# Kernel tuning notes

Hardware: AMD Instinct MI355X
Metric: run time of the kernel (lower is better)

The kernel has to match this reference:

```python
import jax, jax.numpy as jnp
import numpy as np

B, S, HID = 1, 2048, 7168
QLORA = 1536
NH = 32          # index_n_heads
HD = 128         # index_head_dim
ROPE = 64        # qk_rope_head_dim
TOPK = 512       # index_topk
EPS = 1e-6
NEG = -1e9       # finite mask value -> deterministic top-k (no -inf ties)


def _rope(x, cos, sin):
    # non-interleaved rotary: x [b,s,h,d]; cos/sin [s, d//2]
    half = x.shape[-1] // 2
    x1, x2 = x[..., :half], x[..., half:]
    c = cos[None, :, None, :]
    s = sin[None, :, None, :]
    return jnp.concatenate([x1 * c - x2 * s, x1 * s + x2 * c], axis=-1)


def setup_inputs() -> dict:
    key = jax.random.key(0)
    ks = jax.random.split(key, 8)
    x = jax.random.normal(ks[0], (B, S, HID), jnp.float32)
    qr = jax.random.normal(ks[1], (B, S, QLORA), jnp.float32)
    # rotary tables, theta=10000
    inv = 1.0 / (10000.0 ** (np.arange(0, ROPE, 2, dtype=np.float32) / ROPE))
    ang = np.arange(S, dtype=np.float32)[:, None] * inv[None, :]   # [S, ROPE//2]
    freqs_cos = jnp.asarray(np.cos(ang))
    freqs_sin = jnp.asarray(np.sin(ang))
    # causal additive mask [S, S], broadcasts over batch on [b,t,s]
    tri = jnp.tril(jnp.ones((S, S), jnp.bool_))
    mask = jnp.where(tri, 0.0, NEG).astype(jnp.float32)
    wq_b = jax.random.normal(ks[2], (QLORA, NH * HD), jnp.float32) / np.sqrt(QLORA)
    wk = jax.random.normal(ks[3], (HID, HD), jnp.float32) / np.sqrt(HID)
    k_norm_w = jnp.ones((HD,), jnp.float32)
    w_weights = jax.random.normal(ks[4], (HID, NH), jnp.float32) / np.sqrt(HID)
    return {"x": x, "qr": qr, "freqs_cos": freqs_cos, "freqs_sin": freqs_sin,
            "mask": mask, "wq_b": wq_b, "wk": wk, "k_norm_w": k_norm_w,
            "w_weights": w_weights}


def reference(x, qr, freqs_cos, freqs_sin, mask, wq_b, wk, k_norm_w, w_weights):
    b, s, _ = x.shape
    # queries
    q = (qr @ wq_b).reshape(b, s, NH, HD)
    q_pe, q_nope = q[..., :ROPE], q[..., ROPE:]
    q_pe = _rope(q_pe, freqs_cos, freqs_sin)
    q = jnp.concatenate([q_pe, q_nope], axis=-1)            # [b,s,NH,HD]
    # keys: project + RMSNorm + rope on first ROPE dims
    k = x @ wk                                              # [b,s,HD]
    var = jnp.mean(k * k, axis=-1, keepdims=True)
    k = k_norm_w * (k * jax.lax.rsqrt(var + EPS))
    k_pe, k_nope = k[..., :ROPE], k[..., ROPE:]
    k_pe = _rope(k_pe[:, :, None, :], freqs_cos, freqs_sin)[:, :, 0, :]
    k = jnp.concatenate([k_pe, k_nope], axis=-1)            # [b,s,HD]
    # per-head query weights
    weights = (x @ w_weights) * (NH ** -0.5) * (HD ** -0.5)  # [b,s,NH]
    # relu scores and per-head weighted reduction
    logits = jax.nn.relu(jnp.einsum('bthd,bsd->btsh', q, k))  # [b,t,s,NH]
    score = jnp.einsum('btsh,bth->bts', logits, weights) + mask
    # top-k token selection -> additive index mask
    topk_idx = jax.lax.top_k(score, min(TOPK, s))[1]          # [b,t,k]
    bi = jnp.arange(b)[:, None, None]
    ti = jnp.arange(s)[None, :, None]
    out = jnp.full((b, s, s), -jnp.inf, dtype=x.dtype)
    out = out.at[bi, ti, topk_idx].set(0.0)
    return out
```

## Files before the change

kernel.cpp:

```cpp
#include <hip/hip_runtime.h>
#include <hip/hip_bf16.h>
#include <math.h>

#define S_LEN 2048
#define HID   7168
#define QLORA 1536
#define NH    32
#define HD    128
#define T0    512
#define MROWS 1536
#define NEGV  -1000000000.0f
#define EPSV  1e-6f
#define NEG_FILL -3.0e38f
#define KSPLIT 16
#define KCHUNK 448

typedef __attribute__((ext_vector_type(8))) short bf16x8;
typedef __attribute__((ext_vector_type(4))) float f32x4;

__device__ __forceinline__ unsigned short f2bf(float x) {
    __hip_bfloat16 h = __float2bfloat16(x);
    union { __hip_bfloat16 h; unsigned short u; } cv; cv.h = h; return cv.u;
}
__device__ __forceinline__ float bf2f(short u) {
    return __uint_as_float(((unsigned)(unsigned short)u) << 16);
}
__device__ __forceinline__ void gload_lds16(const void* gsrc, void* ldst) {
    __builtin_amdgcn_global_load_lds(
        (const __attribute__((address_space(1))) void*)gsrc,
        (__attribute__((address_space(3))) void*)ldst,
        16, 0, 0);
}

__global__ __launch_bounds__(256) void prep(
    const float* __restrict__ wk, const float* __restrict__ ww,
    const float* __restrict__ wq_b,
    unsigned short* __restrict__ wbT, unsigned short* __restrict__ wqbT)
{
    __shared__ float tbuf[64][65];
    const int tid = threadIdx.x;
    const int b = blockIdx.x;
    if (b < 560) {
        const int k0 = (b % 112) * 64;
        const int nt = b / 112;
        const float* src; int ld, nc0;
        if (nt < 4) { src = wk; ld = HD; nc0 = nt * 32; }
        else        { src = ww; ld = NH; nc0 = 0; }
        {
            int r = tid >> 2, c0 = (tid & 3) * 8;
            const float* sp = &src[(size_t)(k0 + r) * ld + nc0 + c0];
            #pragma unroll
            for (int i = 0; i < 2; ++i) {
                float4 v = *(const float4*)(sp + 4 * i);
                tbuf[r][c0 + 4 * i]     = v.x;
                tbuf[r][c0 + 4 * i + 1] = v.y;
                tbuf[r][c0 + 4 * i + 2] = v.z;
                tbuf[r][c0 + 4 * i + 3] = v.w;
            }
        }
        __syncthreads();
        {
            int nn = tid >> 3, ks = (tid & 7) * 8;
            bf16x8 p;
            #pragma unroll
            for (int j = 0; j < 8; ++j) p[j] = (short)f2bf(tbuf[ks + j][nn]);
            *(bf16x8*)&wbT[(size_t)(nt * 32 + nn) * HID + k0 + ks] = p;
        }
    } else {
        const int b2 = b - 560;
        const int n0 = (b2 & 63) * 64;
        const int k0 = (b2 >> 6) * 64;
        {
            int r = tid >> 2, c0 = (tid & 3) * 16;
            const float* src = &wq_b[(size_t)(k0 + r) * 4096 + n0 + c0];
            #pragma unroll
            for (int i = 0; i < 4; ++i) {
                float4 v = *(const float4*)(src + 4 * i);
                tbuf[r][c0 + 4 * i]     = v.x;
                tbuf[r][c0 + 4 * i + 1] = v.y;
                tbuf[r][c0 + 4 * i + 2] = v.z;
                tbuf[r][c0 + 4 * i + 3] = v.w;
            }
        }
        __syncthreads();
        {
            int nn = tid >> 2, ks = (tid & 3) * 16;
            bf16x8 p0, p1;
            #pragma unroll
            for (int j = 0; j < 8; ++j) {
                p0[j] = (short)f2bf(tbuf[ks + j][nn]);
                p1[j] = (short)f2bf(tbuf[ks + 8 + j][nn]);
            }
            unsigned short* dst = &wqbT[(size_t)(n0 + nn) * QLORA + k0 + ks];
            *(bf16x8*)dst       = p0;
            *(bf16x8*)(dst + 8) = p1;
        }
    }
}

__global__ __launch_bounds__(256) void cast_qr(
    const float* __restrict__ qr, unsigned short* __restrict__ qrb)
{
    int idx = blockIdx.x * 256 + threadIdx.x;
    const float* src = qr + (size_t)T0 * QLORA + (size_t)idx * 8;
    float4 f0 = *(const float4*)src;
    float4 f1 = *(const float4*)(src + 4);
    bf16x8 p;
    p[0]=(short)f2bf(f0.x); p[1]=(short)f2bf(f0.y); p[2]=(short)f2bf(f0.z); p[3]=(short)f2bf(f0.w);
    p[4]=(short)f2bf(f1.x); p[5]=(short)f2bf(f1.y); p[6]=(short)f2bf(f1.z); p[7]=(short)f2bf(f1.w);
    *(bf16x8*)(qrb + (size_t)idx * 8) = p;
}

__global__ __launch_bounds__(256) void kw_gemm2(
    const float* __restrict__ x, const unsigned short* __restrict__ wbT,
    unsigned short* __restrict__ P)
{
    __shared__ char As[2][4096];
    __shared__ char Bs[2][10240];
    const int tid = threadIdx.x;
    const int bid = blockIdx.x;
    const int wg = (bid & 7) * 64 + (bid >> 3);
    const int kc = wg >> 5;
    const int m0 = (wg & 31) * 64;
    const int kbase = kc * KCHUNK;
    const int wv = tid >> 6, l = tid & 63, g = l >> 4, r15 = l & 15;
    const int ar = tid >> 2, asub = tid & 3;
    f32x4 acc[10] = {};
    float4 fa, fb;

#define LOAD_A(kt) do {                                                          \
        const float* ap = &x[(size_t)(m0 + ar) * HID + kbase + (kt) * 32 + asub * 8]; \
        fa = *(const float4*)ap;  fb = *(const float4*)(ap + 4);                 \
    } while (0)
#define WRITE_A(buf) do {                                                        \
        bf16x8 pk;                                                               \
        pk[0]=(short)f2bf(fa.x); pk[1]=(short)f2bf(fa.y);                        \
        pk[2]=(short)f2bf(fa.z); pk[3]=(short)f2bf(fa.w);                        \
        pk[4]=(short)f2bf(fb.x); pk[5]=(short)f2bf(fb.y);                        \
        pk[6]=(short)f2bf(fb.z); pk[7]=(short)f2bf(fb.w);                        \
        *(bf16x8*)(As[buf] + (ar << 6) + ((asub ^ ((ar >> 1) & 3)) << 4)) = pk;  \
    } while (0)
#define STAGE_B(buf, kt) do {                                                    \
        int k0_ = kbase + (kt) * 32;                                             \
        { int slot = (wv << 6) + l;                                              \
          int n_ = slot >> 2, sub_ = (slot & 3) ^ ((n_ >> 1) & 3);               \
          gload_lds16(wbT + (size_t)n_ * HID + k0_ + sub_ * 8,                   \
                      Bs[buf] + (wv << 10)); }                                   \
        { int slot = 256 + (wv << 6) + l;                                        \
          int n_ = slot >> 2, sub_ = (slot & 3) ^ ((n_ >> 1) & 3);               \
          gload_lds16(wbT + (size_t)n_ * HID + k0_ + sub_ * 8,                   \
                      Bs[buf] + 4096 + (wv << 10)); }                            \
        if (wv < 2) {                                                            \
          int slot = 512 + (wv << 6) + l;                                        \
          int n_ = slot >> 2, sub_ = (slot & 3) ^ ((n_ >> 1) & 3);               \
          gload_lds16(wbT + (size_t)n_ * HID + k0_ + sub_ * 8,                   \
                      Bs[buf] + 8192 + (wv << 10)); }                            \
    } while (0)

    LOAD_A(0);
    STAGE_B(0, 0);
    WRITE_A(0);
    __syncthreads();
    int cur = 0;
    for (int t = 0; t < 14; ++t) {
        if (t < 13) { LOAD_A(t + 1); STAGE_B(cur ^ 1, t + 1); }
        {
            char* Ab = As[cur];
            char* Bb = Bs[cur];
            int ra = (wv << 4) + r15;
            bf16x8 a = *(const bf16x8*)(Ab + (ra << 6) + ((g ^ ((ra >> 1) & 3)) << 4));
            #pragma unroll
            for (int fn = 0; fn < 10; ++fn) {
                int nb = (fn << 4) + r15;
                bf16x8 b = *(const bf16x8*)(Bb + (nb << 6) + ((g ^ ((nb >> 1) & 3)) << 4));
                acc[fn] = __builtin_amdgcn_mfma_f32_16x16x32_bf16(a, b, acc[fn], 0, 0, 0);
            }
        }
        if (t < 13) WRITE_A(cur ^ 1);
        __syncthreads();
        cur ^= 1;
    }
#undef LOAD_A
#undef WRITE_A
#undef STAGE_B
    #pragma unroll
    for (int fn = 0; fn < 10; ++fn)
        #pragma unroll
        for (int rr = 0; rr < 4; ++rr) {
            int row = m0 + (wv << 4) + (g << 2) + rr;
            P[((size_t)kc * S_LEN + row) * 160 + (fn << 4) + r15] = f2bf(acc[fn][rr]);
        }
}

__global__ __launch_bounds__(512) void kw_finish16(
    const unsigned short* __restrict__ P, const float* __restrict__ knw,
    const float* __restrict__ fcos, const float* __restrict__ fsin,
    unsigned short* __restrict__ Kf, float* __restrict__ W)
{
    __shared__ float res[16][160];
    __shared__ float rsq[16];
    const int tid = threadIdx.x;
    const int stile = blockIdx.x;
    const int row0 = stile * 16;
    const int r = tid >> 5, j = tid & 31;

    #pragma unroll
    for (int jj = 0; jj < 5; ++jj) {
        int c = j + 32 * jj;
        float s = 0.f;
        #pragma unroll
        for (int kc = 0; kc < KSPLIT; ++kc)
            s += bf2f((short)P[(size_t)(kc * S_LEN + row0 + r) * 160 + c]);
        res[r][c] = s;
    }
    __syncthreads();
    {
        float s2 = 0.f;
        #pragma unroll
        for (int cg = 0; cg < 4; ++cg) { float v = res[r][cg * 32 + j]; s2 += v * v; }
        #pragma unroll
        for (int off = 16; off > 0; off >>= 1) s2 += __shfl_xor(s2, off, 32);
        if (j == 0) rsq[r] = rsqrtf(s2 * (1.0f / 128.0f) + EPSV);
    }
    __syncthreads();
    {
        int rr = tid >> 5, h = tid & 31;
        W[(size_t)(row0 + rr) * NH + h] = res[rr][128 + h] * 0.015625f;
    }
    if (tid < 256) {
        int ks = tid >> 6, l = tid & 63;
        int row = l & 15, g = l >> 4;
        int t = row0 + row;
        float rs = rsq[row];
        bf16x8 pack;
        #pragma unroll
        for (int jj2 = 0; jj2 < 8; ++jj2) {
            int d = ks * 32 + 8 * g + jj2;
            float v;
            if (d < 32) {
                float a = res[row][d]      * rs * knw[d];
                float b = res[row][d + 32] * rs * knw[d + 32];
                v = a * fcos[(size_t)t * 32 + d] - b * fsin[(size_t)t * 32 + d];
            } else if (d < 64) {
                int jx = d - 32;
                float a = res[row][jx] * rs * knw[jx];
                float b = res[row][d]  * rs * knw[d];
                v = a * fsin[(size_t)t * 32 + jx] + b * fcos[(size_t)t * 32 + jx];
            } else {
                v = res[row][d] * rs * knw[d];
            }
            pack[jj2] = (short)f2bf(v);
        }
        *(bf16x8*)&Kf[(size_t)stile * 2048 + ks * 512 + l * 8] = pack;
    }
}

__global__ __launch_bounds__(256) void gemm_q2(
    const unsigned short* __restrict__ qrb, const unsigned short* __restrict__ wqbT,
    const float* __restrict__ fcos, const float* __restrict__ fsin,
    unsigned short* __restrict__ Qbu)
{
    __shared__ char lds[2][12288];
    const int tid = threadIdx.x;
    const int bid = blockIdx.x;
    const int wg = (bid & 7) * 96 + (bid >> 3);
    const int n0 = (wg / 24) * 128;
    const int m0 = (wg % 24) * 64;
    const int wv = tid >> 6, l = tid & 63, g = l >> 4, r15 = l & 15;
    const int lrow = l >> 2, lsub = l & 3;
    const int wm = wv >> 1, wn = wv & 1;
    f32x4 acc[2][4] = {};

#define STAGE_Q(buf, kt) do {                                                   \
        int k0_ = (kt) * 32;                                                    \
        { int row_ = wv * 16 + lrow; int gs_ = lsub ^ ((row_ >> 1) & 3);        \
          gload_lds16(qrb + (size_t)(m0 + row_) * QLORA + k0_ + gs_ * 8,        \
                      lds[buf] + (wv << 10)); }                                 \
        { int row_ = wv * 32 + lrow; int gs_ = lsub ^ ((row_ >> 1) & 3);        \
          gload_lds16(wqbT + (size_t)(n0 + row_) * QLORA + k0_ + gs_ * 8,       \
                      lds[buf] + 4096 + (wv << 11)); }                          \
        { int row_ = wv * 32 + 16 + lrow; int gs_ = lsub ^ ((row_ >> 1) & 3);   \
          gload_lds16(wqbT + (size_t)(n0 + row_) * QLORA + k0_ + gs_ * 8,       \
                      lds[buf] + 4096 + (wv << 11) + 1024); }                   \
    } while (0)

    STAGE_Q(0, 0);
    __syncthreads();
    int cur = 0;
    for (int t = 0; t < 48; ++t) {
        if (t + 1 < 48) STAGE_Q(cur ^ 1, t + 1);
        char* As = lds[cur];
        char* Bs = lds[cur] + 4096;
        bf16x8 a[2], b[4];
        #pragma unroll
        for (int fm = 0; fm < 2; ++fm) {
            int ra = wm * 32 + fm * 16 + r15;
            a[fm] = *(const bf16x8*)(As + (ra << 6) + ((g ^ ((ra >> 1) & 3)) << 4));
        }
        #pragma unroll
        for (int fn = 0; fn < 4; ++fn) {
            int nb = wn * 64 + fn * 16 + r15;
            b[fn] = *(const bf16x8*)(Bs + (nb << 6) + ((g ^ ((nb >> 1) & 3)) << 4));
        }
        #pragma unroll
        for (int fm = 0; fm < 2; ++fm)
            #pragma unroll
            for (int fn = 0; fn < 4; ++fn)
                acc[fm][fn] = __builtin_amdgcn_mfma_f32_16x16x32_bf16(a[fm], b[fn], acc[fm][fn], 0, 0, 0);
        __syncthreads();
        cur ^= 1;
    }
#undef STAGE_Q
    if (wn == 0) {
        #pragma unroll
        for (int fm = 0; fm < 2; ++fm)
            #pragma unroll
            for (int rr = 0; rr < 4; ++rr) {
                int t = T0 + m0 + wm * 32 + fm * 16 + 4 * g + rr;
                #pragma unroll
                for (int p = 0; p < 2; ++p) {
                    int jj = p * 16 + r15;
                    float c = fcos[(size_t)t * 32 + jj];
                    float s = fsin[(size_t)t * 32 + jj];
                    float a = acc[fm][p][rr], b = acc[fm][p + 2][rr];
                    acc[fm][p][rr]     = a * c - b * s;
                    acc[fm][p + 2][rr] = a * s + b * c;
                }
            }
    }
    #pragma unroll
    for (int fm = 0; fm < 2; ++fm)
        #pragma unroll
        for (int fn = 0; fn < 4; ++fn)
            #pragma unroll
            for (int rr = 0; rr < 4; ++rr) {
                int row = m0 + wm * 32 + fm * 16 + 4 * g + rr;
                int col = n0 + wn * 64 + fn * 16 + r15;
                Qbu[(size_t)row * 4096 + col] = f2bf(acc[fm][fn][rr]);
            }
}

__global__ __launch_bounds__(512, 2) void score_mfma3(
    const unsigned short* __restrict__ Qb, const unsigned short* __restrict__ Kf,
    const float* __restrict__ W, float* __restrict__ sc)
{
    __shared__ float ps[2][8][320];
    __shared__ float wl2[32][16];
    const int tid = threadIdx.x;
    const int tt  = 95 - blockIdx.x;
    const int sp  = blockIdx.y;
    const int t0  = T0 + 16 * tt;
    const int wv  = tid >> 6, l = tid & 63, g = l >> 4, r15 = l & 15;

    {
        int h = tid >> 4, gg = (tid >> 2) & 3, r = tid & 3;
        wl2[h][gg * 4 + r] = W[(size_t)(t0 + 4 * gg + r) * NH + h];
    }
    bf16x8 qf[4][4];
    {
        const unsigned short* qbase = Qb + (size_t)(16 * tt + r15) * 4096 + g * 8;
        #pragma unroll
        for (int hh = 0; hh < 4; ++hh)
            #pragma unroll
            for (int ks = 0; ks < 4; ++ks)
                qf[hh][ks] = *(const bf16x8*)(qbase + (4 * wv + hh) * 128 + ks * 32);
    }
    __syncthreads();

    const int nst = 33 + tt;
    bf16x8 kfc[4], kfn[4];
    if (sp < nst) {
        #pragma unroll
        for (int ks = 0; ks < 4; ++ks)
            kfc[ks] = *(const bf16x8*)&Kf[(size_t)sp * 2048 + ks * 512 + l * 8];
    }
    int pb = 0;
    for (int stile = sp; stile < nst; stile += 4) {
        if (stile + 4 < nst) {
            #pragma unroll
            for (int ks = 0; ks < 4; ++ks)
                kfn[ks] = *(const bf16x8*)&Kf[(size_t)(stile + 4) * 2048 + ks * 512 + l * 8];
        }
        f32x4 score = {0.f, 0.f, 0.f, 0.f};
        #pragma unroll
        for (int hh = 0; hh < 4; ++hh) {
            f32x4 acc = {0.f, 0.f, 0.f, 0.f};
            #pragma unroll
            for (int ks = 0; ks < 4; ++ks)
                acc = __builtin_amdgcn_mfma_f32_16x16x32_bf16(qf[hh][ks], kfc[ks], acc, 0, 0, 0);
            f32x4 w4 = *(const f32x4*)&wl2[4 * wv + hh][g * 4];
            #pragma unroll
            for (int r = 0; r < 4; ++r)
                score[r] += fmaxf(acc[r], 0.f) * w4[r];
        }
        #pragma unroll
        for (int r = 0; r < 4; ++r) ps[pb][wv][l * 5 + r] = score[r];
        __syncthreads();
        if (wv < 4) {
            float v = ps[pb][0][l * 5 + wv];
            #pragma unroll
            for (int w = 1; w < 8; ++w) v += ps[pb][w][l * 5 + wv];
            int t = t0 + 4 * g + wv;
            int s = stile * 16 + r15;
            sc[(size_t)(t - T0) * S_LEN + s] = (s <= t) ? v : NEGV;
        }
        #pragma unroll
        for (int ks = 0; ks < 4; ++ks) kfc[ks] = kfn[ks];
        pb ^= 1;
    }
}

__global__ __launch_bounds__(512) void topk_fill(
    const float* __restrict__ sc, float* __restrict__ out)
{
    __shared__ unsigned int hist[8][256];
    __shared__ unsigned int histT[256];
    __shared__ unsigned int wtot[8];
    __shared__ unsigned int sh_prefix;
    __shared__ int sh_krem;
    const int tid = threadIdx.x;
    if (blockIdx.x >= MROWS) {
        int idx = (blockIdx.x - MROWS) * 512 + tid;
        int col4 = idx & 511;
        float v = (col4 < 128) ? 0.0f : NEG_FILL;
        float4 o = {v, v, v, v};
        ((float4*)out)[idx] = o;
        return;
    }
    const int lane = tid & 63, wvi = tid >> 6;
    const int qrow = blockIdx.x;
    const int t = T0 + qrow;

    unsigned int uv[4];
    {
        float4 v = ((const float4*)(sc + (size_t)qrow * S_LEN))[tid];
        float vv[4] = {v.x, v.y, v.z, v.w};
        #pragma unroll
        for (int jj = 0; jj < 4; ++jj) {
            int i = tid * 4 + jj;
            float f = (i <= t) ? vv[jj] : NEGV;
            unsigned int b = __float_as_uint(f);
            uv[jj] = (b & 0x80000000u) ? ~b : (b | 0x80000000u);
        }
    }
    if (tid == 0) { sh_prefix = 0u; sh_krem = 512; }
    __syncthreads();

    #pragma unroll
    for (int pass = 0; pass < 4; ++pass) {
        const int shift = 24 - 8 * pass;
        ((unsigned int*)hist)[tid] = 0u;
        ((unsigned int*)hist)[tid + 512] = 0u;
        ((unsigned int*)hist)[tid + 1024] = 0u;
        ((unsigned int*)hist)[tid + 1536] = 0u;
        __syncthreads();
        unsigned int pfx = sh_prefix;
        #pragma unroll
        for (int jj = 0; jj < 4; ++jj) {
            bool ok = (pass == 0) || ((uv[jj] >> (shift + 8)) == (pfx >> (shift + 8)));
            if (ok) atomicAdd(&hist[wvi][(uv[jj] >> shift) & 255u], 1u);
        }
        __syncthreads();
        int krem = sh_krem;
        if (tid < 256) {
            unsigned int v = 0u;
            #pragma unroll
            for (int w = 0; w < 8; ++w) v += hist[w][tid];
            unsigned int s = v;
            #pragma unroll
            for (int off = 1; off < 64; off <<= 1) {
                unsigned int t2 = __shfl_down(s, off, 64);
                if (lane + off < 64) s += t2;
            }
            if (lane == 0) wtot[wvi] = s;
            histT[tid] = v;
        }
        __syncthreads();
        if (tid < 256) {
            unsigned int v = histT[tid];
            unsigned int s = v;
            #pragma unroll
            for (int off = 1; off < 64; off <<= 1) {
                unsigned int t2 = __shfl_down(s, off, 64);
                if (lane + off < 64) s += t2;
            }
            unsigned int S = s;
            #pragma unroll
            for (int w = 0; w < 4; ++w)
                if (w > wvi) S += wtot[w];
            if ((int)S >= krem && (int)(S - v) < krem) {
                sh_krem = krem - (int)(S - v);
                sh_prefix = pfx | ((unsigned int)tid << shift);
            }
        }
        __syncthreads();
    }

    const unsigned int uthr = sh_prefix;
    const int krem = sh_krem;
    int ec = 0;
    #pragma unroll
    for (int jj = 0; jj < 4; ++jj) ec += (uv[jj] == uthr) ? 1 : 0;
    unsigned int c = (unsigned int)ec;
    unsigned int p = c;
    #pragma unroll
    for (int off = 1; off < 64; off <<= 1) {
        unsigned int t2 = __shfl_up(p, off, 64);
        if (lane >= off) p += t2;
    }
    if (lane == 63) wtot[wvi] = p;
    __syncthreads();
    unsigned int add = 0;
    #pragma unroll
    for (int w = 0; w < 8; ++w)
        if (w < wvi) add += wtot[w];
    int base = (int)(p - c + add);

    float o[4];
    #pragma unroll
    for (int jj = 0; jj < 4; ++jj) {
        unsigned int u = uv[jj];
        bool sel;
        if (u > uthr) { sel = true; }
        else if (u == uthr) { sel = (base < krem); base++; }
        else { sel = false; }
        o[jj] = sel ? 0.0f : NEG_FILL;
    }
    float4 ov = {o[0], o[1], o[2], o[3]};
    ((float4*)(out + (size_t)t * S_LEN))[tid] = ov;
}

extern "C" void kernel_launch(void* const* d_in, const int* in_sizes, int n_in,
                              void* d_out, int out_size, void* d_ws, size_t ws_size,
                              hipStream_t stream)
{
    (void)in_sizes; (void)n_in; (void)out_size; (void)ws_size;
    const float* x    = (const float*)d_in[0];
    const float* qr   = (const float*)d_in[1];
    const float* fcos = (const float*)d_in[2];
    const float* fsin = (const float*)d_in[3];
    const float* wq_b = (const float*)d_in[5];
    const float* wk   = (const float*)d_in[6];
    const float* knw  = (const float*)d_in[7];
    const float* ww   = (const float*)d_in[8];
    float* out = (float*)d_out;
    char*  wsb = (char*)d_ws;

    unsigned short* Kf   = (unsigned short*)wsb;
    float*          W    = (float*)(wsb + 512 * 1024);
    unsigned short* wbT  = (unsigned short*)(wsb + 768 * 1024);
    unsigned short* wqbT = (unsigned short*)(wsb + 3080192);
    float*          sc   = (float*)(wsb + 3080192);
    unsigned short* qrb  = (unsigned short*)(wsb + 15663104);
    unsigned short* P    = (unsigned short*)(wsb + 15663104);
    unsigned short* Qbu  = (unsigned short*)d_out;

    prep        <<<2096, 256,        0, stream>>>(wk, ww, wq_b, wbT, wqbT);
    cast_qr     <<<1152, 256,        0, stream>>>(qr, qrb);
    gemm_q2     <<<768, 256,         0, stream>>>(qrb, wqbT, fcos, fsin, Qbu);
    kw_gemm2    <<<512, 256,         0, stream>>>(x, wbT, P);
    kw_finish16 <<<128, 512,         0, stream>>>(P, knw, fcos, fsin, Kf, W);
    score_mfma3 <<<dim3(96, 4), 512, 0, stream>>>(Qbu, Kf, W, sc);
    topk_fill   <<<2048, 512,        0, stream>>>(sc, out);
}
```

Measured before the change: 148.5 us.

## Triple-buffer Q-projection GEMM with manual vmcnt waits and single barrier

Converts the gemm_q2 main loop from double-buffered LDS staging with two syncthreads per step to a three-stage ring buffer. Each step uses explicit s_waitcnt vmcnt(3) plus one raw s_barrier, so two tiles of global-to-LDS loads stay in flight while the current one is computed. Global and LDS addresses are precomputed outside the loop and the loop is unrolled by three. This adds LDS (36KB per block) and may reduce occupancy, and it depends on precise vmcnt counting for correctness.

```diff
diff --git a/kernel.cpp b/kernel.cpp
--- a/kernel.cpp
+++ b/kernel.cpp
@@ -260,7 +260,7 @@
     const float* __restrict__ fcos, const float* __restrict__ fsin,
     unsigned short* __restrict__ Qbu)
 {
-    __shared__ char lds[2][12288];
+    __shared__ char lds[3][12288];
     const int tid = threadIdx.x;
     const int bid = blockIdx.x;
     const int wg = (bid & 7) * 96 + (bid >> 3);
@@ -271,46 +271,71 @@
     const int wm = wv >> 1, wn = wv & 1;
     f32x4 acc[2][4] = {};
 
-#define STAGE_Q(buf, kt) do {                                                   \
-        int k0_ = (kt) * 32;                                                    \
-        { int row_ = wv * 16 + lrow; int gs_ = lsub ^ ((row_ >> 1) & 3);        \
-          gload_lds16(qrb + (size_t)(m0 + row_) * QLORA + k0_ + gs_ * 8,        \
-                      lds[buf] + (wv << 10)); }                                 \
-        { int row_ = wv * 32 + lrow; int gs_ = lsub ^ ((row_ >> 1) & 3);        \
-          gload_lds16(wqbT + (size_t)(n0 + row_) * QLORA + k0_ + gs_ * 8,       \
-                      lds[buf] + 4096 + (wv << 11)); }                          \
-        { int row_ = wv * 32 + 16 + lrow; int gs_ = lsub ^ ((row_ >> 1) & 3);   \
-          gload_lds16(wqbT + (size_t)(n0 + row_) * QLORA + k0_ + gs_ * 8,       \
-                      lds[buf] + 4096 + (wv << 11) + 1024); }                   \
+    const int rowq = wv * 16 + lrow;
+    const char* gq  = (const char*)(qrb + (size_t)(m0 + rowq) * QLORA
+                                    + (lsub ^ ((rowq >> 1) & 3)) * 8);
+    const int  ldq  = wv << 10;
+    const int rowb1 = wv * 32 + lrow;
+    const char* gb1 = (const char*)(wqbT + (size_t)(n0 + rowb1) * QLORA
+                                    + (lsub ^ ((rowb1 >> 1) & 3)) * 8);
+    const int  ldb1 = 4096 + (wv << 11);
+    const int rowb2 = wv * 32 + 16 + lrow;
+    const char* gb2 = (const char*)(wqbT + (size_t)(n0 + rowb2) * QLORA
+                                    + (lsub ^ ((rowb2 >> 1) & 3)) * 8);
+    const int  ldb2 = 4096 + (wv << 11) + 1024;
+
+    const int ra0 = wm * 32 + r15,      ra1 = wm * 32 + 16 + r15;
+    const int offA0 = (ra0 << 6) + ((g ^ ((ra0 >> 1) & 3)) << 4);
+    const int offA1 = (ra1 << 6) + ((g ^ ((ra1 >> 1) & 3)) << 4);
+    const int nb0 = wn * 64 + r15,      nb1 = wn * 64 + 16 + r15;
+    const int nb2 = wn * 64 + 32 + r15, nb3 = wn * 64 + 48 + r15;
+    const int offB0 = 4096 + (nb0 << 6) + ((g ^ ((nb0 >> 1) & 3)) << 4);
+    const int offB1 = 4096 + (nb1 << 6) + ((g ^ ((nb1 >> 1) & 3)) << 4);
+    const int offB2 = 4096 + (nb2 << 6) + ((g ^ ((nb2 >> 1) & 3)) << 4);
+    const int offB3 = 4096 + (nb3 << 6) + ((g ^ ((nb3 >> 1) & 3)) << 4);
+
+#define STAGE3(bufi, kt) do {                                                   \
+        int kb = (kt) * 64;                                                     \
+        gload_lds16(gq  + kb, lds[bufi] + ldq);                                 \
+        gload_lds16(gb1 + kb, lds[bufi] + ldb1);                                \
+        gload_lds16(gb2 + kb, lds[bufi] + ldb2);                                \
     } while (0)
-
-    STAGE_Q(0, 0);
-    __syncthreads();
-    int cur = 0;
-    for (int t = 0; t < 48; ++t) {
-        if (t + 1 < 48) STAGE_Q(cur ^ 1, t + 1);
-        char* As = lds[cur];
-        char* Bs = lds[cur] + 4096;
-        bf16x8 a[2], b[4];
-        #pragma unroll
-        for (int fm = 0; fm < 2; ++fm) {
-            int ra = wm * 32 + fm * 16 + r15;
-            a[fm] = *(const bf16x8*)(As + (ra << 6) + ((g ^ ((ra >> 1) & 3)) << 4));
-        }
-        #pragma unroll
-        for (int fn = 0; fn < 4; ++fn) {
-            int nb = wn * 64 + fn * 16 + r15;
-            b[fn] = *(const bf16x8*)(Bs + (nb << 6) + ((g ^ ((nb >> 1) & 3)) << 4));
-        }
-        #pragma unroll
-        for (int fm = 0; fm < 2; ++fm)
-            #pragma unroll
-            for (int fn = 0; fn < 4; ++fn)
-                acc[fm][fn] = __builtin_amdgcn_mfma_f32_16x16x32_bf16(a[fm], b[fn], acc[fm][fn], 0, 0, 0);
-        __syncthreads();
-        cur ^= 1;
-    }
-#undef STAGE_Q
+#define COMPUTE(bufi) do {                                                      \
+        char* L_ = lds[bufi];                                                   \
+        bf16x8 a0 = *(const bf16x8*)(L_ + offA0);                               \
+        bf16x8 a1 = *(const bf16x8*)(L_ + offA1);                               \
+        bf16x8 b0_ = *(const bf16x8*)(L_ + offB0);                              \
+        bf16x8 b1_ = *(const bf16x8*)(L_ + offB1);                              \
+        bf16x8 b2_ = *(const bf16x8*)(L_ + offB2);                              \
+        bf16x8 b3_ = *(const bf16x8*)(L_ + offB3);                              \
+        acc[0][0] = __builtin_amdgcn_mfma_f32_16x16x32_bf16(a0, b0_, acc[0][0], 0, 0, 0); \
+        acc[0][1] = __builtin_amdgcn_mfma_f32_16x16x32_bf16(a0, b1_, acc[0][1], 0, 0, 0); \
+        acc[0][2] = __builtin_amdgcn_mfma_f32_16x16x32_bf16(a0, b2_, acc[0][2], 0, 0, 0); \
+        acc[0][3] = __builtin_amdgcn_mfma_f32_16x16x32_bf16(a0, b3_, acc[0][3], 0, 0, 0); \
+        acc[1][0] = __builtin_amdgcn_mfma_f32_16x16x32_bf16(a1, b0_, acc[1][0], 0, 0, 0); \
+        acc[1][1] = __builtin_amdgcn_mfma_f32_16x16x32_bf16(a1, b1_, acc[1][1], 0, 0, 0); \
+        acc[1][2] = __builtin_amdgcn_mfma_f32_16x16x32_bf16(a1, b2_, acc[1][2], 0, 0, 0); \
+        acc[1][3] = __builtin_amdgcn_mfma_f32_16x16x32_bf16(a1, b3_, acc[1][3], 0, 0, 0); \
+    } while (0)
+#define WAITV3 asm volatile("s_waitcnt vmcnt(3)" ::: "memory")
+#define WAITV0 asm volatile("s_waitcnt vmcnt(0)" ::: "memory")
+#define BAR    __builtin_amdgcn_s_barrier()
+
+    STAGE3(0, 0);
+    STAGE3(1, 1);
+    for (int t = 0; t < 45; t += 3) {
+        WAITV3; BAR; STAGE3(2, t + 2); COMPUTE(0);
+        WAITV3; BAR; STAGE3(0, t + 3); COMPUTE(1);
+        WAITV3; BAR; STAGE3(1, t + 4); COMPUTE(2);
+    }
+    WAITV3; BAR; STAGE3(2, 47); COMPUTE(0);
+    WAITV3; BAR; COMPUTE(1);
+    WAITV0; BAR; COMPUTE(2);
+#undef STAGE3
+#undef COMPUTE
+#undef WAITV3
+#undef WAITV0
+#undef BAR
     if (wn == 0) {
         #pragma unroll
         for (int fm = 0; fm < 2; ++fm)
```

New measurement: 147.2 us. Within noise of the previous version (-0.9%).

## Merge Q and K GEMMs into one launch, fuse qr cast, tweak score occupancy

Applied to the files above, without the earlier changes.

Combines the query GEMM and the key/weights GEMM into a single kernel whose blocks branch on block index, so both run concurrently in one launch. The separate qr fp32-to-bf16 cast kernel is removed; the query GEMM now loads fp32 qr and converts it in registers before writing to LDS, removing a kernel and a round trip through global memory. The score kernel switches to an explicit waves-per-EU attribute, loads the Q fragments with inline asm, and adds a sched_barrier. The shared LDS union sets occupancy for both halves, and the in-register conversion adds VALU work inside the Q GEMM loop.

```diff
diff --git a/kernel.cpp b/kernel.cpp
--- a/kernel.cpp
+++ b/kernel.cpp
@@ -98,98 +98,193 @@
     }
 }
 
-__global__ __launch_bounds__(256) void cast_qr(
-    const float* __restrict__ qr, unsigned short* __restrict__ qrb)
-{
-    int idx = blockIdx.x * 256 + threadIdx.x;
-    const float* src = qr + (size_t)T0 * QLORA + (size_t)idx * 8;
-    float4 f0 = *(const float4*)src;
-    float4 f1 = *(const float4*)(src + 4);
-    bf16x8 p;
-    p[0]=(short)f2bf(f0.x); p[1]=(short)f2bf(f0.y); p[2]=(short)f2bf(f0.z); p[3]=(short)f2bf(f0.w);
-    p[4]=(short)f2bf(f1.x); p[5]=(short)f2bf(f1.y); p[6]=(short)f2bf(f1.z); p[7]=(short)f2bf(f1.w);
-    *(bf16x8*)(qrb + (size_t)idx * 8) = p;
-}
-
-__global__ __launch_bounds__(256) void kw_gemm2(
+__global__ __launch_bounds__(256) void gemms(
+    const float* __restrict__ qr, const unsigned short* __restrict__ wqbT,
+    const float* __restrict__ fcos, const float* __restrict__ fsin,
+    unsigned short* __restrict__ Qbu,
     const float* __restrict__ x, const unsigned short* __restrict__ wbT,
     unsigned short* __restrict__ P)
 {
-    __shared__ char As[2][4096];
-    __shared__ char Bs[2][10240];
+    __shared__ char ldsu[28672];
     const int tid = threadIdx.x;
     const int bid = blockIdx.x;
-    const int wg = (bid & 7) * 64 + (bid >> 3);
-    const int kc = wg >> 5;
-    const int m0 = (wg & 31) * 64;
-    const int kbase = kc * KCHUNK;
     const int wv = tid >> 6, l = tid & 63, g = l >> 4, r15 = l & 15;
-    const int ar = tid >> 2, asub = tid & 3;
-    f32x4 acc[10] = {};
-    float4 fa, fb;
-
-#define LOAD_A(kt) do {                                                          \
-        const float* ap = &x[(size_t)(m0 + ar) * HID + kbase + (kt) * 32 + asub * 8]; \
+
+    if (bid < 768) {
+        const int wg = (bid & 7) * 96 + (bid >> 3);
+        const int n0 = (wg / 24) * 128;
+        const int m0 = (wg % 24) * 64;
+        const int wm = wv >> 1, wn = wv & 1;
+        const int ar = tid >> 2, asub = tid & 3;
+        f32x4 acc[2][4] = {};
+        float4 fa, fb;
+
+#define QA(buf)      (ldsu + (buf) * 4096)
+#define QB(buf)      (ldsu + 8192 + (buf) * 8192)
+#define LOAD_AQ(kt) do {                                                         \
+        const float* ap = &qr[(size_t)(T0 + m0 + ar) * QLORA + (kt) * 32 + asub * 8]; \
         fa = *(const float4*)ap;  fb = *(const float4*)(ap + 4);                 \
     } while (0)
-#define WRITE_A(buf) do {                                                        \
+#define WRITE_AQ(buf) do {                                                       \
         bf16x8 pk;                                                               \
         pk[0]=(short)f2bf(fa.x); pk[1]=(short)f2bf(fa.y);                        \
         pk[2]=(short)f2bf(fa.z); pk[3]=(short)f2bf(fa.w);                        \
         pk[4]=(short)f2bf(fb.x); pk[5]=(short)f2bf(fb.y);                        \
         pk[6]=(short)f2bf(fb.z); pk[7]=(short)f2bf(fb.w);                        \
-        *(bf16x8*)(As[buf] + (ar << 6) + ((asub ^ ((ar >> 1) & 3)) << 4)) = pk;  \
+        *(bf16x8*)(QA(buf) + (ar << 6) + ((asub ^ ((ar >> 1) & 3)) << 4)) = pk;  \
     } while (0)
-#define STAGE_B(buf, kt) do {                                                    \
+#define STAGE_BQ(buf, kt) do {                                                   \
+        int k0_ = (kt) * 32;                                                     \
+        { int slot = (wv << 6) + l;                                              \
+          int n_ = slot >> 2, sub_ = (slot & 3) ^ ((n_ >> 1) & 3);               \
+          gload_lds16(wqbT + (size_t)(n0 + n_) * QLORA + k0_ + sub_ * 8,         \
+                      QB(buf) + (wv << 10)); }                                   \
+        { int slot = 256 + (wv << 6) + l;                                        \
+          int n_ = slot >> 2, sub_ = (slot & 3) ^ ((n_ >> 1) & 3);               \
+          gload_lds16(wqbT + (size_t)(n0 + n_) * QLORA + k0_ + sub_ * 8,         \
+                      QB(buf) + 4096 + (wv << 10)); }                            \
+    } while (0)
+
+        LOAD_AQ(0);
+        STAGE_BQ(0, 0);
+        WRITE_AQ(0);
+        __syncthreads();
+        int cur = 0;
+        for (int t = 0; t < 48; ++t) {
+            if (t + 1 < 48) { LOAD_AQ(t + 1); STAGE_BQ(cur ^ 1, t + 1); }
+            {
+                char* Ab = QA(cur);
+                char* Bb = QB(cur);
+                bf16x8 a[2], b[4];
+                #pragma unroll
+                for (int fm = 0; fm < 2; ++fm) {
+                    int ra = wm * 32 + fm * 16 + r15;
+                    a[fm] = *(const bf16x8*)(Ab + (ra << 6) + ((g ^ ((ra >> 1) & 3)) << 4));
+                }
+                #pragma unroll
+                for (int fn = 0; fn < 4; ++fn) {
+                    int nb = wn * 64 + fn * 16 + r15;
+                    b[fn] = *(const bf16x8*)(Bb + (nb << 6) + ((g ^ ((nb >> 1) & 3)) << 4));
+                }
+                #pragma unroll
+                for (int fm = 0; fm < 2; ++fm)
+                    #pragma unroll
+                    for (int fn = 0; fn < 4; ++fn)
+                        acc[fm][fn] = __builtin_amdgcn_mfma_f32_16x16x32_bf16(a[fm], b[fn], acc[fm][fn], 0, 0, 0);
+            }
+            if (t + 1 < 48) WRITE_AQ(cur ^ 1);
+            __syncthreads();
+            cur ^= 1;
+        }
+#undef QA
+#undef QB
+#undef LOAD_AQ
+#undef WRITE_AQ
+#undef STAGE_BQ
+        if (wn == 0) {
+            #pragma unroll
+            for (int fm = 0; fm < 2; ++fm)
+                #pragma unroll
+                for (int rr = 0; rr < 4; ++rr) {
+                    int t = T0 + m0 + wm * 32 + fm * 16 + 4 * g + rr;
+                    #pragma unroll
+                    for (int p = 0; p < 2; ++p) {
+                        int jj = p * 16 + r15;
+                        float c = fcos[(size_t)t * 32 + jj];
+                        float s = fsin[(size_t)t * 32 + jj];
+                        float a = acc[fm][p][rr], b = acc[fm][p + 2][rr];
+                        acc[fm][p][rr]     = a * c - b * s;
+                        acc[fm][p + 2][rr] = a * s + b * c;
+                    }
+                }
+        }
+        #pragma unroll
+        for (int fm = 0; fm < 2; ++fm)
+            #pragma unroll
+            for (int fn = 0; fn < 4; ++fn)
+                #pragma unroll
+                for (int rr = 0; rr < 4; ++rr) {
+                    int row = m0 + wm * 32 + fm * 16 + 4 * g + rr;
+                    int col = n0 + wn * 64 + fn * 16 + r15;
+                    Qbu[(size_t)row * 4096 + col] = f2bf(acc[fm][fn][rr]);
+                }
+    } else {
+        const int bid2 = bid - 768;
+        const int wg = (bid2 & 7) * 64 + (bid2 >> 3);
+        const int kc = wg >> 5;
+        const int m0 = (wg & 31) * 64;
+        const int kbase = kc * KCHUNK;
+        const int ar = tid >> 2, asub = tid & 3;
+        f32x4 acc[10] = {};
+        float4 fa, fb;
+
+#define KA(buf)      (ldsu + (buf) * 4096)
+#define KB(buf)      (ldsu + 8192 + (buf) * 10240)
+#define LOAD_AK(kt) do {                                                         \
+        const float* ap = &x[(size_t)(m0 + ar) * HID + kbase + (kt) * 32 + asub * 8]; \
+        fa = *(const float4*)ap;  fb = *(const float4*)(ap + 4);                 \
+    } while (0)
+#define WRITE_AK(buf) do {                                                       \
+        bf16x8 pk;                                                               \
+        pk[0]=(short)f2bf(fa.x); pk[1]=(short)f2bf(fa.y);                        \
+        pk[2]=(short)f2bf(fa.z); pk[3]=(short)f2bf(fa.w);                        \
+        pk[4]=(short)f2bf(fb.x); pk[5]=(short)f2bf(fb.y);                        \
+        pk[6]=(short)f2bf(fb.z); pk[7]=(short)f2bf(fb.w);                        \
+        *(bf16x8*)(KA(buf) + (ar << 6) + ((asub ^ ((ar >> 1) & 3)) << 4)) = pk;  \
+    } while (0)
+#define STAGE_BK(buf, kt) do {                                                   \
         int k0_ = kbase + (kt) * 32;                                             \
         { int slot = (wv << 6) + l;                                              \
           int n_ = slot >> 2, sub_ = (slot & 3) ^ ((n_ >> 1) & 3);               \
           gload_lds16(wbT + (size_t)n_ * HID + k0_ + sub_ * 8,                   \
-                      Bs[buf] + (wv << 10)); }                                   \
+                      KB(buf) + (wv << 10)); }                                   \
         { int slot = 256 + (wv << 6) + l;                                        \
           int n_ = slot >> 2, sub_ = (slot & 3) ^ ((n_ >> 1) & 3);               \
           gload_lds16(wbT + (size_t)n_ * HID + k0_ + sub_ * 8,                   \
-                      Bs[buf] + 4096 + (wv << 10)); }                            \
+                      KB(buf) + 4096 + (wv << 10)); }                            \
         if (wv < 2) {                                                            \
           int slot = 512 + (wv << 6) + l;                                        \
           int n_ = slot >> 2, sub_ = (slot & 3) ^ ((n_ >> 1) & 3);               \
           gload_lds16(wbT + (size_t)n_ * HID + k0_ + sub_ * 8,                   \
-                      Bs[buf] + 8192 + (wv << 10)); }                            \
+                      KB(buf) + 8192 + (wv << 10)); }                            \
     } while (0)
 
-    LOAD_A(0);
-    STAGE_B(0, 0);
-    WRITE_A(0);
-    __syncthreads();
-    int cur = 0;
-    for (int t = 0; t < 14; ++t) {
-        if (t < 13) { LOAD_A(t + 1); STAGE_B(cur ^ 1, t + 1); }
-        {
-            char* Ab = As[cur];
-            char* Bb = Bs[cur];
-            int ra = (wv << 4) + r15;
-            bf16x8 a = *(const bf16x8*)(Ab + (ra << 6) + ((g ^ ((ra >> 1) & 3)) << 4));
-            #pragma unroll
-            for (int fn = 0; fn < 10; ++fn) {
-                int nb = (fn << 4) + r15;
-                bf16x8 b = *(const bf16x8*)(Bb + (nb << 6) + ((g ^ ((nb >> 1) & 3)) << 4));
-                acc[fn] = __builtin_amdgcn_mfma_f32_16x16x32_bf16(a, b, acc[fn], 0, 0, 0);
-            }
-        }
-        if (t < 13) WRITE_A(cur ^ 1);
-        __syncthreads();
-        cur ^= 1;
-    }
-#undef LOAD_A
-#undef WRITE_A
-#undef STAGE_B
-    #pragma unroll
-    for (int fn = 0; fn < 10; ++fn)
-        #pragma unroll
-        for (int rr = 0; rr < 4; ++rr) {
-            int row = m0 + (wv << 4) + (g << 2) + rr;
-            P[((size_t)kc * S_LEN + row) * 160 + (fn << 4) + r15] = f2bf(acc[fn][rr]);
-        }
+        LOAD_AK(0);
+        STAGE_BK(0, 0);
+        WRITE_AK(0);
+        __syncthreads();
+        int cur = 0;
+        for (int t = 0; t < 14; ++t) {
+            if (t < 13) { LOAD_AK(t + 1); STAGE_BK(cur ^ 1, t + 1); }
+            {
+                char* Ab = KA(cur);
+                char* Bb = KB(cur);
+                int ra = (wv << 4) + r15;
+                bf16x8 a = *(const bf16x8*)(Ab + (ra << 6) + ((g ^ ((ra >> 1) & 3)) << 4));
+                #pragma unroll
+                for (int fn = 0; fn < 10; ++fn) {
+                    int nb = (fn << 4) + r15;
+                    bf16x8 b = *(const bf16x8*)(Bb + (nb << 6) + ((g ^ ((nb >> 1) & 3)) << 4));
+                    acc[fn] = __builtin_amdgcn_mfma_f32_16x16x32_bf16(a, b, acc[fn], 0, 0, 0);
+                }
+            }
+            if (t < 13) WRITE_AK(cur ^ 1);
+            __syncthreads();
+            cur ^= 1;
+        }
+#undef KA
+#undef KB
+#undef LOAD_AK
+#undef WRITE_AK
+#undef STAGE_BK
+        #pragma unroll
+        for (int fn = 0; fn < 10; ++fn)
+            #pragma unroll
+            for (int rr = 0; rr < 4; ++rr) {
+                int row = m0 + (wv << 4) + (g << 2) + rr;
+                P[((size_t)kc * S_LEN + row) * 160 + (fn << 4) + r15] = f2bf(acc[fn][rr]);
+            }
+    }
 }
 
 __global__ __launch_bounds__(512) void kw_finish16(
@@ -255,92 +350,9 @@
     }
 }
 
-__global__ __launch_bounds__(256) void gemm_q2(
-    const unsigned short* __restrict__ qrb, const unsigned short* __restrict__ wqbT,
-    const float* __restrict__ fcos, const float* __restrict__ fsin,
-    unsigned short* __restrict__ Qbu)
-{
-    __shared__ char lds[2][12288];
-    const int tid = threadIdx.x;
-    const int bid = blockIdx.x;
-    const int wg = (bid & 7) * 96 + (bid >> 3);
-    const int n0 = (wg / 24) * 128;
-    const int m0 = (wg % 24) * 64;
-    const int wv = tid >> 6, l = tid & 63, g = l >> 4, r15 = l & 15;
-    const int lrow = l >> 2, lsub = l & 3;
-    const int wm = wv >> 1, wn = wv & 1;
-    f32x4 acc[2][4] = {};
-
-#define STAGE_Q(buf, kt) do {                                                   \
-        int k0_ = (kt) * 32;                                                    \
-        { int row_ = wv * 16 + lrow; int gs_ = lsub ^ ((row_ >> 1) & 3);        \
-          gload_lds16(qrb + (size_t)(m0 + row_) * QLORA + k0_ + gs_ * 8,        \
-                      lds[buf] + (wv << 10)); }                                 \
-        { int row_ = wv * 32 + lrow; int gs_ = lsub ^ ((row_ >> 1) & 3);        \
-          gload_lds16(wqbT + (size_t)(n0 + row_) * QLORA + k0_ + gs_ * 8,       \
-                      lds[buf] + 4096 + (wv << 11)); }                          \
-        { int row_ = wv * 32 + 16 + lrow; int gs_ = lsub ^ ((row_ >> 1) & 3);   \
-          gload_lds16(wqbT + (size_t)(n0 + row_) * QLORA + k0_ + gs_ * 8,       \
-                      lds[buf] + 4096 + (wv << 11) + 1024); }                   \
-    } while (0)
-
-    STAGE_Q(0, 0);
-    __syncthreads();
-    int cur = 0;
-    for (int t = 0; t < 48; ++t) {
-        if (t + 1 < 48) STAGE_Q(cur ^ 1, t + 1);
-        char* As = lds[cur];
-        char* Bs = lds[cur] + 4096;
-        bf16x8 a[2], b[4];
-        #pragma unroll
-        for (int fm = 0; fm < 2; ++fm) {
-            int ra = wm * 32 + fm * 16 + r15;
-            a[fm] = *(const bf16x8*)(As + (ra << 6) + ((g ^ ((ra >> 1) & 3)) << 4));
-        }
-        #pragma unroll
-        for (int fn = 0; fn < 4; ++fn) {
-            int nb = wn * 64 + fn * 16 + r15;
-            b[fn] = *(const bf16x8*)(Bs + (nb << 6) + ((g ^ ((nb >> 1) & 3)) << 4));
-        }
-        #pragma unroll
-        for (int fm = 0; fm < 2; ++fm)
-            #pragma unroll
-            for (int fn = 0; fn < 4; ++fn)
-                acc[fm][fn] = __builtin_amdgcn_mfma_f32_16x16x32_bf16(a[fm], b[fn], acc[fm][fn], 0, 0, 0);
-        __syncthreads();
-        cur ^= 1;
-    }
-#undef STAGE_Q
-    if (wn == 0) {
-        #pragma unroll
-        for (int fm = 0; fm < 2; ++fm)
-            #pragma unroll
-            for (int rr = 0; rr < 4; ++rr) {
-                int t = T0 + m0 + wm * 32 + fm * 16 + 4 * g + rr;
-                #pragma unroll
-                for (int p = 0; p < 2; ++p) {
-                    int jj = p * 16 + r15;
-                    float c = fcos[(size_t)t * 32 + jj];
-                    float s = fsin[(size_t)t * 32 + jj];
-                    float a = acc[fm][p][rr], b = acc[fm][p + 2][rr];
-                    acc[fm][p][rr]     = a * c - b * s;
-                    acc[fm][p + 2][rr] = a * s + b * c;
-                }
-            }
-    }
-    #pragma unroll
-    for (int fm = 0; fm < 2; ++fm)
-        #pragma unroll
-        for (int fn = 0; fn < 4; ++fn)
-            #pragma unroll
-            for (int rr = 0; rr < 4; ++rr) {
-                int row = m0 + wm * 32 + fm * 16 + 4 * g + rr;
-                int col = n0 + wn * 64 + fn * 16 + r15;
-                Qbu[(size_t)row * 4096 + col] = f2bf(acc[fm][fn][rr]);
-            }
-}
-
-__global__ __launch_bounds__(512, 2) void score_mfma3(
+__global__ __launch_bounds__(512)
+__attribute__((amdgpu_waves_per_eu(4, 4)))
+void score_mfma3(
     const unsigned short* __restrict__ Qb, const unsigned short* __restrict__ Kf,
     const float* __restrict__ W, float* __restrict__ sc)
 {
@@ -362,10 +374,14 @@
         #pragma unroll
         for (int hh = 0; hh < 4; ++hh)
             #pragma unroll
-            for (int ks = 0; ks < 4; ++ks)
-                qf[hh][ks] = *(const bf16x8*)(qbase + (4 * wv + hh) * 128 + ks * 32);
+            for (int ks = 0; ks < 4; ++ks) {
+                const unsigned short* ap = qbase + (4 * wv + hh) * 128 + ks * 32;
+                asm volatile("global_load_dwordx4 %0, %1, off"
+                             : "=v"(qf[hh][ks]) : "v"(ap) : "memory");
+            }
     }
     __syncthreads();
+    __builtin_amdgcn_sched_barrier(0);
 
     const int nst = 33 + tt;
     bf16x8 kfc[4], kfn[4];
@@ -551,14 +567,11 @@
     unsigned short* wbT  = (unsigned short*)(wsb + 768 * 1024);
     unsigned short* wqbT = (unsigned short*)(wsb + 3080192);
     float*          sc   = (float*)(wsb + 3080192);
-    unsigned short* qrb  = (unsigned short*)(wsb + 15663104);
     unsigned short* P    = (unsigned short*)(wsb + 15663104);
     unsigned short* Qbu  = (unsigned short*)d_out;
 
     prep        <<<2096, 256,        0, stream>>>(wk, ww, wq_b, wbT, wqbT);
-    cast_qr     <<<1152, 256,        0, stream>>>(qr, qrb);
-    gemm_q2     <<<768, 256,         0, stream>>>(qrb, wqbT, fcos, fsin, Qbu);
-    kw_gemm2    <<<512, 256,         0, stream>>>(x, wbT, P);
+    gemms       <<<1280, 256,        0, stream>>>(qr, wqbT, fcos, fsin, Qbu, x, wbT, P);
     kw_finish16 <<<128, 512,         0, stream>>>(P, knw, fcos, fsin, Kf, W);
     score_mfma3 <<<dim3(96, 4), 512, 0, stream>>>(Qbu, Kf, W, sc);
     topk_fill   <<<2048, 512,        0, stream>>>(sc, out);
```

Result: no change. 145.6 us (-1.9%).
